# Kernel tuning notes

Hardware: AMD Instinct MI355X
Metric: run time of the kernel (lower is better)

Reference implementation:

```python
import jax, jax.numpy as jnp
import numpy as np

D_MODEL = 1024
N_HEADS = 16
D_K = D_MODEL // N_HEADS
D_FF = 4096
B = 2
T = 2048


def _layernorm(x, gamma, beta, eps=1e-5):
    mu = jnp.mean(x, axis=-1, keepdims=True)
    var = jnp.var(x, axis=-1, keepdims=True)
    return (x - mu) * jax.lax.rsqrt(var + eps) * gamma + beta


def _attention(q_in, kv_in, Wq, bq, Wk, bk, Wv, bv, mask):
    # q_in: [B,Tq,D], kv_in: [B,Tk,D]; Wq/Wk/Wv: [H,D,d_k]; b*: [H,d_k]
    Q = jnp.einsum('btd,hdk->bhtk', q_in, Wq) + bq[None, :, None, :]
    K = jnp.einsum('bsd,hdk->bhsk', kv_in, Wk) + bk[None, :, None, :]
    V = jnp.einsum('bsd,hdk->bhsk', kv_in, Wv) + bv[None, :, None, :]
    scores = jnp.einsum('bhtk,bhsk->bhts', Q, K) / jnp.sqrt(jnp.asarray(D_K, Q.dtype))
    if mask is not None:
        scores = jnp.where(mask, scores, jnp.finfo(scores.dtype).min)
    attn = jax.nn.softmax(scores, axis=-1)
    out = jnp.einsum('bhts,bhsk->bhtk', attn, V)  # [B,H,Tq,d_k]
    # concat heads: [B,Tq,H*d_k] == [B,Tq,D]
    return out.transpose(0, 2, 1, 3).reshape(q_in.shape[0], q_in.shape[1], -1)


def setup_inputs() -> dict:
    key = jax.random.key(0)
    ks = jax.random.split(key, 24)
    s = 0.02
    inp = {
        'dec_input': jax.random.normal(ks[0], (B, T, D_MODEL), jnp.float32),
        'enc_output': jax.random.normal(ks[1], (B, T, D_MODEL), jnp.float32),
        # self-attention per-head weights stacked over heads
        'Wq_s': jax.random.normal(ks[2], (N_HEADS, D_MODEL, D_K), jnp.float32) * s,
        'bq_s': jnp.zeros((N_HEADS, D_K), jnp.float32),
        'Wk_s': jax.random.normal(ks[3], (N_HEADS, D_MODEL, D_K), jnp.float32) * s,
        'bk_s': jnp.zeros((N_HEADS, D_K), jnp.float32),
        'Wv_s': jax.random.normal(ks[4], (N_HEADS, D_MODEL, D_K), jnp.float32) * s,
        'bv_s': jnp.zeros((N_HEADS, D_K), jnp.float32),
        'Wo_s': jax.random.normal(ks[5], (D_MODEL, D_MODEL), jnp.float32) * s,
        'bo_s': jnp.zeros((D_MODEL,), jnp.float32),
        # cross-attention per-head weights
        'Wq_c': jax.random.normal(ks[6], (N_HEADS, D_MODEL, D_K), jnp.float32) * s,
        'bq_c': jnp.zeros((N_HEADS, D_K), jnp.float32),
        'Wk_c': jax.random.normal(ks[7], (N_HEADS, D_MODEL, D_K), jnp.float32) * s,
        'bk_c': jnp.zeros((N_HEADS, D_K), jnp.float32),
        'Wv_c': jax.random.normal(ks[8], (N_HEADS, D_MODEL, D_K), jnp.float32) * s,
        'bv_c': jnp.zeros((N_HEADS, D_K), jnp.float32),
        'Wo_c': jax.random.normal(ks[9], (D_MODEL, D_MODEL), jnp.float32) * s,
        'bo_c': jnp.zeros((D_MODEL,), jnp.float32),
        # FFN
        'W1': jax.random.normal(ks[10], (D_MODEL, D_FF), jnp.float32) * s,
        'b1': jnp.zeros((D_FF,), jnp.float32),
        'W2': jax.random.normal(ks[11], (D_FF, D_MODEL), jnp.float32) * s,
        'b2': jnp.zeros((D_MODEL,), jnp.float32),
        # layernorms
        'g1': jnp.ones((D_MODEL,), jnp.float32), 'be1': jnp.zeros((D_MODEL,), jnp.float32),
        'g2': jnp.ones((D_MODEL,), jnp.float32), 'be2': jnp.zeros((D_MODEL,), jnp.float32),
        'g3': jnp.ones((D_MODEL,), jnp.float32), 'be3': jnp.zeros((D_MODEL,), jnp.float32),
    }
    return inp


def reference(dec_input, enc_output,
              Wq_s, bq_s, Wk_s, bk_s, Wv_s, bv_s, Wo_s, bo_s,
              Wq_c, bq_c, Wk_c, bk_c, Wv_c, bv_c, Wo_c, bo_c,
              W1, b1, W2, b2, g1, be1, g2, be2, g3, be3):
    Tq = dec_input.shape[1]
    causal = jnp.tril(jnp.ones((Tq, Tq), bool))[None, None, :, :]  # [1,1,T,T]
    # masked multi-head self-attention (dropout is identity in eval)
    sa = _attention(dec_input, dec_input, Wq_s, bq_s, Wk_s, bk_s, Wv_s, bv_s, causal)
    sa = sa @ Wo_s.T if False else jnp.einsum('btd,ed->bte', sa, Wo_s.T) if False else sa @ Wo_s + bo_s
    x1 = _layernorm(dec_input + sa, g1, be1)
    # cross-attention (no mask)
    ca = _attention(x1, enc_output, Wq_c, bq_c, Wk_c, bk_c, Wv_c, bv_c, None)
    ca = ca @ Wo_c + bo_c
    x2 = _layernorm(x1 + ca, g2, be2)
    # FFN
    ffn = jax.nn.relu(x2 @ W1 + b1) @ W2 + b2
    x3 = _layernorm(x2 + ffn, g3, be3)
    return x3
```

## Files before the change

kernel.cpp:

```cpp
#include <hip/hip_runtime.h>
#include <hip/hip_bf16.h>

typedef __attribute__((ext_vector_type(8))) short short8;
typedef __attribute__((ext_vector_type(4))) short short4v;
typedef __attribute__((ext_vector_type(4))) float floatx4;

#define TDIM 2048
#define BDIM 2
#define MROWS (BDIM * TDIM)

#define ASM_VMCNT0() __asm__ volatile("s_waitcnt vmcnt(0)" ::: "memory")
#define ASM_LGKM0()  __asm__ volatile("s_waitcnt lgkmcnt(0)" ::: "memory")
#define ASM_BARRIER() __asm__ volatile("s_barrier" ::: "memory")

__device__ __forceinline__ floatx4 mfma16(short4v a, short4v b, floatx4 c) {
#if defined(__HIP_DEVICE_COMPILE__)
#if __has_builtin(__builtin_amdgcn_mfma_f32_16x16x16bf16_1k)
    return __builtin_amdgcn_mfma_f32_16x16x16bf16_1k(a, b, c, 0, 0, 0);
#else
    short8 az = {a[0], a[1], a[2], a[3], 0, 0, 0, 0};
    short8 bz = {b[0], b[1], b[2], b[3], 0, 0, 0, 0};
    return __builtin_amdgcn_mfma_f32_16x16x32_bf16(az, bz, c, 0, 0, 0);
#endif
#else
    (void)a; (void)b;
    return c;
#endif
}

__device__ __forceinline__ void gload_lds16(const void* g, void* l) {
    __builtin_amdgcn_global_load_lds((const __attribute__((address_space(1))) void*)g,
                                     (__attribute__((address_space(3))) void*)l, 16, 0, 0);
}

__device__ __forceinline__ short bf16s(float x) {
    __hip_bfloat16 h = __float2bfloat16(x);
    return *(short*)&h;
}

__global__ __launch_bounds__(256) void cast2_k(const float* __restrict__ a,
                                               const float* __restrict__ b,
                                               __hip_bfloat16* __restrict__ oa,
                                               __hip_bfloat16* __restrict__ ob) {
    const int blk = blockIdx.x;
    const float* in = (blk < 4096) ? a : b;
    __hip_bfloat16* out = (blk < 4096) ? oa : ob;
    const size_t base = (size_t)(blk & 4095) * 1024 + threadIdx.x * 4;
    float4 v = *(const float4*)&in[base];
    out[base + 0] = __float2bfloat16(v.x);
    out[base + 1] = __float2bfloat16(v.y);
    out[base + 2] = __float2bfloat16(v.z);
    out[base + 3] = __float2bfloat16(v.w);
}

__device__ __forceinline__ void t32(float (*tile)[33], const float* __restrict__ in,
                                    __hip_bfloat16* __restrict__ out, int R, int C,
                                    int c0, int r0) {
    const int tx = threadIdx.x & 31, ty = threadIdx.x >> 5;
#pragma unroll
    for (int i = 0; i < 4; ++i)
        tile[ty + 8 * i][tx] = in[(size_t)(r0 + ty + 8 * i) * C + c0 + tx];
    __syncthreads();
#pragma unroll
    for (int i = 0; i < 4; ++i)
        out[(size_t)(c0 + ty + 8 * i) * R + r0 + tx] = __float2bfloat16(tile[tx][ty + 8 * i]);
}

__global__ __launch_bounds__(256) void prep_w_k(
    const float* __restrict__ Wq_s, const float* __restrict__ Wk_s, const float* __restrict__ Wv_s,
    const float* __restrict__ Wq_c, const float* __restrict__ Wk_c, const float* __restrict__ Wv_c,
    const float* __restrict__ Wo_s, const float* __restrict__ Wo_c,
    const float* __restrict__ W1, const float* __restrict__ W2,
    const float* __restrict__ bq_s, const float* __restrict__ bk_s, const float* __restrict__ bv_s,
    const float* __restrict__ bk_c, const float* __restrict__ bv_c,
    __hip_bfloat16* __restrict__ WtQKVs, __hip_bfloat16* __restrict__ WtQc,
    __hip_bfloat16* __restrict__ WtKVc, __hip_bfloat16* __restrict__ WtOs,
    __hip_bfloat16* __restrict__ WtOc, __hip_bfloat16* __restrict__ Wt1,
    __hip_bfloat16* __restrict__ Wt2,
    float* __restrict__ BiasQKVs, float* __restrict__ BiasKVc) {
    __shared__ float tile[32][33];
    const int t = blockIdx.x;
    if (t < 6144) {
        const int seg = t >> 10, tl = t & 1023;
        const float* s;
        __hip_bfloat16* d;
        if (seg == 0) { s = Wq_s; d = WtQKVs; }
        else if (seg == 1) { s = Wk_s; d = WtQKVs + 1048576; }
        else if (seg == 2) { s = Wv_s; d = WtQKVs + 2097152; }
        else if (seg == 3) { s = Wq_c; d = WtQc; }
        else if (seg == 4) { s = Wk_c; d = WtKVc; }
        else { s = Wv_c; d = WtKVc + 1048576; }
        const int slab = tl >> 6, rem = tl & 63;
        t32(tile, s + (size_t)slab * 65536, d + (size_t)slab * 65536, 1024, 64,
            (rem & 1) * 32, (rem >> 1) * 32);
    } else if (t < 8192) {
        const int rem = (t - 6144) & 1023;
        const float* s = (t < 7168) ? Wo_s : Wo_c;
        __hip_bfloat16* d = (t < 7168) ? WtOs : WtOc;
        t32(tile, s, d, 1024, 1024, (rem & 31) * 32, (rem >> 5) * 32);
    } else if (t < 12288) {
        const int rem = t - 8192;
        t32(tile, W1, Wt1, 1024, 4096, (rem & 127) * 32, (rem >> 7) * 32);
    } else if (t < 16384) {
        const int rem = t - 12288;
        t32(tile, W2, Wt2, 4096, 1024, (rem & 31) * 32, (rem >> 5) * 32);
    } else if (t < 16396) {
        const int i = (t - 16384) * 256 + threadIdx.x;
        BiasQKVs[i] = (i < 1024) ? bq_s[i] : (i < 2048 ? bk_s[i - 1024] : bv_s[i - 2048]);
    } else {
        const int i = (t - 16396) * 256 + threadIdx.x;
        BiasKVc[i] = (i < 1024) ? bk_c[i] : bv_c[i - 1024];
    }
}

__device__ __forceinline__ void gemm_core(
    const __hip_bfloat16* __restrict__ A, const __hip_bfloat16* __restrict__ Bt,
    int K, int kBeg, int kLen,
    const float* __restrict__ bias, __hip_bfloat16* __restrict__ C, int ldc,
    float* __restrict__ Pf,
    __hip_bfloat16* __restrict__ Vt, int vt_col0, int relu,
    int m0, int n0, __hip_bfloat16* sm) {
    const int tid = threadIdx.x;
    const int lane = tid & 63, wave = tid >> 6;
    const int quad = lane >> 4, l16 = lane & 15;
    const int wm = (wave >> 1) * 64, wn = (wave & 1) * 64;
    const int lrow = lane >> 3;
    const int gsw = (((lane & 7) ^ lrow)) * 8;
    const int sw7 = l16 & 7;
    const __hip_bfloat16* gA = A + (size_t)(m0 + wave * 32 + lrow) * K + kBeg + gsw;
    const __hip_bfloat16* gB = Bt + (size_t)(n0 + wave * 32 + lrow) * K + kBeg + gsw;
    __hip_bfloat16* lA = sm + wave * 2048;
    __hip_bfloat16* lB = sm + 16384 + wave * 2048;
    floatx4 acc[4][4] = {};
    const int T = kLen >> 6;
#pragma unroll
    for (int i = 0; i < 4; ++i) {
        gload_lds16(gA + (size_t)i * 8 * K, lA + i * 512);
        gload_lds16(gB + (size_t)i * 8 * K, lB + i * 512);
    }
    for (int t = 0; t < T; ++t) {
        ASM_VMCNT0();
        ASM_BARRIER();
        if (t + 1 < T) {
            const int koff = (t + 1) << 6;
            const int b = ((t + 1) & 1) * 8192;
#pragma unroll
            for (int i = 0; i < 4; ++i) {
                gload_lds16(gA + (size_t)i * 8 * K + koff, lA + b + i * 512);
                gload_lds16(gB + (size_t)i * 8 * K + koff, lB + b + i * 512);
            }
        }
        const __hip_bfloat16* cA = sm + (t & 1) * 8192;
        const __hip_bfloat16* cB = sm + 16384 + (t & 1) * 8192;
#pragma unroll
        for (int kc = 0; kc < 2; ++kc) {
            short8 af[4], bfr[4];
#pragma unroll
            for (int i = 0; i < 4; ++i) {
                af[i] = *(const short8*)&cA[(wm + i * 16 + l16) * 64 +
                                            (((kc * 4 + quad) ^ sw7) * 8)];
                bfr[i] = *(const short8*)&cB[(wn + i * 16 + l16) * 64 +
                                             (((kc * 4 + quad) ^ sw7) * 8)];
            }
#pragma unroll
            for (int mi = 0; mi < 4; ++mi)
#pragma unroll
                for (int ni = 0; ni < 4; ++ni)
                    acc[mi][ni] =
                        __builtin_amdgcn_mfma_f32_16x16x32_bf16(af[mi], bfr[ni], acc[mi][ni], 0, 0, 0);
        }
    }
    if (Pf) {
#pragma unroll
        for (int ni = 0; ni < 4; ++ni) {
            const int col = n0 + wn + ni * 16 + l16;
#pragma unroll
            for (int mi = 0; mi < 4; ++mi)
#pragma unroll
                for (int r = 0; r < 4; ++r) {
                    const int row = m0 + wm + mi * 16 + quad * 4 + r;
                    Pf[(size_t)row * ldc + col] = acc[mi][ni][r];
                }
        }
    } else {
        const bool toVt = (n0 >= vt_col0);
#pragma unroll
        for (int ni = 0; ni < 4; ++ni) {
            const int col = n0 + wn + ni * 16 + l16;
            const float bv = bias[col];
#pragma unroll
            for (int mi = 0; mi < 4; ++mi) {
                const int row0 = m0 + wm + mi * 16 + quad * 4;
                if (toVt) {
                    const int b = row0 >> 11, t0 = row0 & (TDIM - 1);
                    short4v pk;
#pragma unroll
                    for (int r = 0; r < 4; ++r) pk[r] = bf16s(acc[mi][ni][r] + bv);
                    *(short4v*)&Vt[((size_t)(b * 1024 + (col - vt_col0)) << 11) + t0] = pk;
                } else {
#pragma unroll
                    for (int r = 0; r < 4; ++r) {
                        float v = acc[mi][ni][r] + bv;
                        if (relu) v = fmaxf(v, 0.f);
                        C[(size_t)(row0 + r) * ldc + col] = __float2bfloat16(v);
                    }
                }
            }
        }
    }
}

__global__ __launch_bounds__(256) void gemm_bf16_k(const __hip_bfloat16* __restrict__ A,
                                                   const __hip_bfloat16* __restrict__ Bt,
                                                   const float* __restrict__ bias,
                                                   __hip_bfloat16* __restrict__ C,
                                                   int N, int K, int relu,
                                                   __hip_bfloat16* __restrict__ Vt, int vt_col0) {
    __shared__ __hip_bfloat16 sm[2 * 128 * 64 * 2];
    gemm_core(A, Bt, K, 0, K, bias, C, N, nullptr, Vt, vt_col0, relu,
              blockIdx.y * 128, blockIdx.x * 128, sm);
}

__global__ __launch_bounds__(256) void gemm_sk2_k(const __hip_bfloat16* __restrict__ A,
                                                  const __hip_bfloat16* __restrict__ Bt,
                                                  float* __restrict__ Pf, int N, int K) {
    __shared__ __hip_bfloat16 sm[2 * 128 * 64 * 2];
    const int z = blockIdx.z;
    gemm_core(A, Bt, K, z * (K >> 1), K >> 1, nullptr, nullptr, N,
              Pf + (size_t)z * MROWS * N, nullptr, 1 << 30, 0,
              blockIdx.y * 128, blockIdx.x * 128, sm);
}

__global__ __launch_bounds__(256) void gemm_pair_k(
    const __hip_bfloat16* __restrict__ A1, const __hip_bfloat16* __restrict__ Bt1,
    const float* __restrict__ bias1, __hip_bfloat16* __restrict__ C1, int N1, int K1,
    const __hip_bfloat16* __restrict__ A2, const __hip_bfloat16* __restrict__ Bt2,
    const float* __restrict__ bias2, __hip_bfloat16* __restrict__ C2, int N2, int K2,
    __hip_bfloat16* __restrict__ Vt2, int vtc2, int nx1) {
    __shared__ __hip_bfloat16 sm[2 * 128 * 64 * 2];
    if ((int)blockIdx.x < nx1)
        gemm_core(A1, Bt1, K1, 0, K1, bias1, C1, N1, nullptr, nullptr, 1 << 30, 0,
                  blockIdx.y * 128, blockIdx.x * 128, sm);
    else
        gemm_core(A2, Bt2, K2, 0, K2, bias2, C2, N2, nullptr, Vt2, vtc2, 0,
                  blockIdx.y * 128, (blockIdx.x - nx1) * 128, sm);
}

__device__ __forceinline__ void flash_one(
    const __hip_bfloat16* __restrict__ Q, int ldq, int qc0,
    const __hip_bfloat16* __restrict__ Kp, int ldk,
    const __hip_bfloat16* __restrict__ Vp,
    __hip_bfloat16* __restrict__ O, int causal, int q0, size_t rowb, int h,
    __hip_bfloat16* sK, __hip_bfloat16* sV) {
    const int tid = threadIdx.x, lane = tid & 63, wave = tid >> 6;
    const int quad = lane >> 4, l16 = lane & 15;
    const int lrow = lane >> 3;
    const int gsw = ((lane & 7) ^ lrow) * 8;
    const int sw7 = l16 & 7;
    short8 qf[2];
    {
        const __hip_bfloat16* qp = Q + (rowb + q0 + wave * 16 + l16) * (size_t)ldq + qc0 + h * 64;
        const float qs = 0.18033688f;
        short8 r0 = *(const short8*)(qp + quad * 8);
        short8 r1 = *(const short8*)(qp + 32 + quad * 8);
#pragma unroll
        for (int j = 0; j < 8; ++j) {
            qf[0][j] = bf16s(__uint_as_float(((unsigned)(unsigned short)r0[j]) << 16) * qs);
            qf[1][j] = bf16s(__uint_as_float(((unsigned)(unsigned short)r1[j]) << 16) * qs);
        }
    }
    short4v ones4;
#pragma unroll
    for (int j = 0; j < 4; ++j) ones4[j] = (short)0x3F80;
    floatx4 Ot[4] = {};
    floatx4 accl = {};
    const int nDiag = q0 >> 6;
    const int lastT = causal ? nDiag : (TDIM >> 6) - 1;
    ASM_LGKM0();
    ASM_BARRIER();
#pragma unroll
    for (int i = 0; i < 2; ++i) {
        const int rb = wave * 16 + i * 8;
        gload_lds16(&Kp[(rowb + rb + lrow) * (size_t)ldk + gsw], &sK[rb * 64]);
        gload_lds16(&Vp[(size_t)(rb + lrow) * TDIM + gsw], &sV[rb * 64]);
    }
    for (int t = 0; t <= lastT; ++t) {
        ASM_VMCNT0();
        ASM_BARRIER();
        if (t < lastT) {
            const int s1 = (t + 1) << 6, nb = ((t + 1) & 1) * 4096;
#pragma unroll
            for (int i = 0; i < 2; ++i) {
                const int rb = wave * 16 + i * 8;
                gload_lds16(&Kp[(rowb + s1 + rb + lrow) * (size_t)ldk + gsw], &sK[nb + rb * 64]);
                gload_lds16(&Vp[(size_t)(rb + lrow) * TDIM + s1 + gsw], &sV[nb + rb * 64]);
            }
        }
        const int cb = (t & 1) * 4096;
        floatx4 Sf[4] = {};
#pragma unroll
        for (int st = 0; st < 4; ++st) {
            short8 b0 = *(const short8*)&sK[cb + (st * 16 + l16) * 64 + ((quad ^ sw7) * 8)];
            short8 b1 = *(const short8*)&sK[cb + (st * 16 + l16) * 64 + (((4 + quad) ^ sw7) * 8)];
            Sf[st] = __builtin_amdgcn_mfma_f32_16x16x32_bf16(b0, qf[0], Sf[st], 0, 0, 0);
            Sf[st] = __builtin_amdgcn_mfma_f32_16x16x32_bf16(b1, qf[1], Sf[st], 0, 0, 0);
        }
#pragma unroll
        for (int st = 0; st < 4; ++st)
#pragma unroll
            for (int r = 0; r < 4; ++r) Sf[st][r] = exp2f(Sf[st][r]);
        if (causal && t == nDiag) {
            const int qr = wave * 16 + l16;
#pragma unroll
            for (int st = 0; st < 4; ++st)
#pragma unroll
                for (int r = 0; r < 4; ++r)
                    if (st * 16 + quad * 4 + r > qr) Sf[st][r] = 0.f;
        }
        short4v pf[4];
#pragma unroll
        for (int st = 0; st < 4; ++st)
#pragma unroll
            for (int r = 0; r < 4; ++r) pf[st][r] = bf16s(Sf[st][r]);
#pragma unroll
        for (int st = 0; st < 4; ++st) accl = mfma16(ones4, pf[st], accl);
#pragma unroll
        for (int dt = 0; dt < 4; ++dt)
#pragma unroll
            for (int st = 0; st < 4; ++st) {
                short4v av = *(const short4v*)&sV[cb + (dt * 16 + l16) * 64 +
                                                 (((st * 2 + (quad >> 1)) ^ sw7) * 8) +
                                                 (quad & 1) * 4];
                Ot[dt] = mfma16(av, pf[st], Ot[dt]);
            }
    }
    const float inv = 1.0f / accl[0];
    __hip_bfloat16* op = O + (rowb + q0 + wave * 16 + l16) * (size_t)1024 + h * 64 + quad * 4;
#pragma unroll
    for (int dt = 0; dt < 4; ++dt) {
        short4v pk;
#pragma unroll
        for (int r = 0; r < 4; ++r) pk[r] = bf16s(Ot[dt][r] * inv);
        *(short4v*)(op + dt * 16) = pk;
    }
}

__global__ __launch_bounds__(256) void flash_attn(const __hip_bfloat16* __restrict__ Q, int ldq, int qc0,
                                                  const __hip_bfloat16* __restrict__ K, int ldk, int kc0,
                                                  const __hip_bfloat16* __restrict__ Vt,
                                                  __hip_bfloat16* __restrict__ O, int causal) {
    __shared__ __hip_bfloat16 sK[2 * 64 * 64];
    __shared__ __hip_bfloat16 sV[2 * 64 * 64];
    const int bh = blockIdx.y, b = bh >> 4, h = bh & 15;
    const size_t rowb = (size_t)b * TDIM;
    const __hip_bfloat16* Kp = K + kc0 + h * 64;
    const __hip_bfloat16* Vp = Vt + ((size_t)(b * 1024 + h * 64) << 11);
    if (causal) {
        flash_one(Q, ldq, qc0, Kp, ldk, Vp, O, 1, (31 - (int)blockIdx.x) * 64, rowb, h, sK, sV);
    } else {
        flash_one(Q, ldq, qc0, Kp, ldk, Vp, O, 0, (int)blockIdx.x * 64, rowb, h, sK, sV);
    }
}

__global__ __launch_bounds__(256) void ln2_k(const float* __restrict__ resid,
                                             const float* __restrict__ d0,
                                             const float* __restrict__ d1,
                                             const float* __restrict__ biasN,
                                             const float* __restrict__ gamma,
                                             const float* __restrict__ beta,
                                             float* __restrict__ outf,
                                             __hip_bfloat16* __restrict__ outb) {
    const int row = blockIdx.x, tid = threadIdx.x;
    const size_t base = (size_t)row * 1024;
    float x[4], s = 0.f, sq = 0.f;
#pragma unroll
    for (int i = 0; i < 4; ++i) {
        const int c = tid + 256 * i;
        x[i] = resid[base + c] + d0[base + c] + d1[base + c] + biasN[c];
        s += x[i];
        sq += x[i] * x[i];
    }
#pragma unroll
    for (int off = 32; off > 0; off >>= 1) {
        s += __shfl_down(s, off);
        sq += __shfl_down(sq, off);
    }
    __shared__ float red[8];
    if ((tid & 63) == 0) {
        red[tid >> 6] = s;
        red[4 + (tid >> 6)] = sq;
    }
    __syncthreads();
    const float S = red[0] + red[1] + red[2] + red[3];
    const float Q2 = red[4] + red[5] + red[6] + red[7];
    const float mean = S * (1.f / 1024.f);
    const float var = Q2 * (1.f / 1024.f) - mean * mean;
    const float rstd = rsqrtf(var + 1e-5f);
#pragma unroll
    for (int i = 0; i < 4; ++i) {
        const int c = tid + 256 * i;
        const float y = (x[i] - mean) * rstd * gamma[c] + beta[c];
        outf[base + c] = y;
        if (outb) outb[base + c] = __float2bfloat16(y);
    }
}

extern "C" void kernel_launch(void* const* d_in, const int* in_sizes, int n_in,
                              void* d_out, int out_size, void* d_ws, size_t ws_size,
                              hipStream_t stream) {
    (void)in_sizes; (void)n_in; (void)out_size; (void)ws_size;
    const float* dec  = (const float*)d_in[0];
    const float* enc  = (const float*)d_in[1];
    const float* Wq_s = (const float*)d_in[2];
    const float* bq_s = (const float*)d_in[3];
    const float* Wk_s = (const float*)d_in[4];
    const float* bk_s = (const float*)d_in[5];
    const float* Wv_s = (const float*)d_in[6];
    const float* bv_s = (const float*)d_in[7];
    const float* Wo_s = (const float*)d_in[8];
    const float* bo_s = (const float*)d_in[9];
    const float* Wq_c = (const float*)d_in[10];
    const float* bq_c = (const float*)d_in[11];
    const float* Wk_c = (const float*)d_in[12];
    const float* bk_c = (const float*)d_in[13];
    const float* Wv_c = (const float*)d_in[14];
    const float* bv_c = (const float*)d_in[15];
    const float* Wo_c = (const float*)d_in[16];
    const float* bo_c = (const float*)d_in[17];
    const float* W1   = (const float*)d_in[18];
    const float* b1   = (const float*)d_in[19];
    const float* W2   = (const float*)d_in[20];
    const float* b2   = (const float*)d_in[21];
    const float* g1   = (const float*)d_in[22];
    const float* be1  = (const float*)d_in[23];
    const float* g2   = (const float*)d_in[24];
    const float* be2  = (const float*)d_in[25];
    const float* g3   = (const float*)d_in[26];
    const float* be3  = (const float*)d_in[27];

    char* w = (char*)d_ws;
    const size_t MB = 1ull << 20;
    __hip_bfloat16* Xdec   = (__hip_bfloat16*)(w + 0 * MB);
    __hip_bfloat16* Xenc   = (__hip_bfloat16*)(w + 8 * MB);
    __hip_bfloat16* WtQKVs = (__hip_bfloat16*)(w + 16 * MB);
    __hip_bfloat16* WtOs   = (__hip_bfloat16*)(w + 22 * MB);
    __hip_bfloat16* WtQc   = (__hip_bfloat16*)(w + 24 * MB);
    __hip_bfloat16* WtKVc  = (__hip_bfloat16*)(w + 26 * MB);
    __hip_bfloat16* WtOc   = (__hip_bfloat16*)(w + 30 * MB);
    __hip_bfloat16* Wt1    = (__hip_bfloat16*)(w + 32 * MB);
    __hip_bfloat16* Wt2    = (__hip_bfloat16*)(w + 40 * MB);
    float*          BiasQKVs = (float*)(w + 48 * MB);
    float*          BiasKVc  = (float*)(w + 48 * MB + 65536);
    __hip_bfloat16* QKV    = (__hip_bfloat16*)(w + 49 * MB);
    __hip_bfloat16* Qc     = QKV;
    __hip_bfloat16* KVc    = (__hip_bfloat16*)(w + 57 * MB);
    float*          Psplit = (float*)(w + 49 * MB);
    __hip_bfloat16* VtBuf  = (__hip_bfloat16*)(w + 73 * MB);
    __hip_bfloat16* Attn   = (__hip_bfloat16*)(w + 81 * MB);
    float*          X1f    = (float*)(w + 97 * MB);
    __hip_bfloat16* X1b    = (__hip_bfloat16*)(w + 113 * MB);
    float*          X2f    = (float*)(w + 121 * MB);
    __hip_bfloat16* X2b    = (__hip_bfloat16*)(w + 137 * MB);
    __hip_bfloat16* H1     = (__hip_bfloat16*)(w + 145 * MB);
    float*          P0     = Psplit;
    float*          P1     = Psplit + (size_t)MROWS * 1024;
    const int NOVT = 1 << 30;

    cast2_k<<<8192, 256, 0, stream>>>(dec, enc, Xdec, Xenc);
    prep_w_k<<<16404, 256, 0, stream>>>(Wq_s, Wk_s, Wv_s, Wq_c, Wk_c, Wv_c, Wo_s, Wo_c,
                                        W1, W2, bq_s, bk_s, bv_s, bk_c, bv_c,
                                        WtQKVs, WtQc, WtKVc, WtOs, WtOc, Wt1, Wt2,
                                        BiasQKVs, BiasKVc);

    gemm_bf16_k<<<dim3(24, 32), 256, 0, stream>>>(Xdec, WtQKVs, BiasQKVs, QKV, 3072, 1024, 0,
                                                  VtBuf, 2048);
    flash_attn<<<dim3(32, 32), 256, 0, stream>>>(QKV, 3072, 0, QKV, 3072, 1024, VtBuf, Attn, 1);
    gemm_sk2_k<<<dim3(8, 32, 2), 256, 0, stream>>>(Attn, WtOs, Psplit, 1024, 1024);
    ln2_k<<<MROWS, 256, 0, stream>>>(dec, P0, P1, bo_s, g1, be1, X1f, X1b);

    gemm_pair_k<<<dim3(24, 32), 256, 0, stream>>>(X1b, WtQc, bq_c, Qc, 1024, 1024,
                                                  Xenc, WtKVc, BiasKVc, KVc, 2048, 1024,
                                                  VtBuf, 1024, 8);
    flash_attn<<<dim3(32, 32), 256, 0, stream>>>(Qc, 1024, 0, KVc, 2048, 0, VtBuf, Attn, 0);
    gemm_sk2_k<<<dim3(8, 32, 2), 256, 0, stream>>>(Attn, WtOc, Psplit, 1024, 1024);
    ln2_k<<<MROWS, 256, 0, stream>>>(X1f, P0, P1, bo_c, g2, be2, X2f, X2b);

    gemm_bf16_k<<<dim3(32, 32), 256, 0, stream>>>(X2b, Wt1, b1, H1, 4096, 1024, 1,
                                                  (__hip_bfloat16*)nullptr, NOVT);
    gemm_sk2_k<<<dim3(8, 32, 2), 256, 0, stream>>>(H1, Wt2, Psplit, 1024, 4096);
    ln2_k<<<MROWS, 256, 0, stream>>>(X2f, P0, P1, b2, g3, be3, (float*)d_out, (__hip_bfloat16*)nullptr);
}
```

Measured before the change: 553.5 us.

## Split long causal attention query tiles across two blocks with combine kernel

For causal self-attention, query tiles 16..31 (the longest KV ranges) are each split into two halves of the KV loop, run as separate blocks writing fp32 partial outputs and row sums, then merged by a new combine kernel. This balances per-block work across the grid (48 blocks per head instead of 32) to cut the tail of the causal triangle. It also swaps exp2f for the hardware exp2 builtin. The cost is extra partial-buffer traffic and an additional kernel launch. The split needs no max rescaling because the softmax here is unnormalised and uses no running max.

```diff
diff --git a/kernel.cpp b/kernel.cpp
--- a/kernel.cpp
+++ b/kernel.cpp
@@ -36,6 +36,18 @@
 __device__ __forceinline__ short bf16s(float x) {
     __hip_bfloat16 h = __float2bfloat16(x);
     return *(short*)&h;
+}
+
+__device__ __forceinline__ float fexp2(float x) {
+#if defined(__HIP_DEVICE_COMPILE__)
+#if __has_builtin(__builtin_amdgcn_exp2f)
+    return __builtin_amdgcn_exp2f(x);
+#else
+    return exp2f(x);
+#endif
+#else
+    return x;
+#endif
 }
 
 __global__ __launch_bounds__(256) void cast2_k(const float* __restrict__ a,
@@ -251,6 +263,7 @@
     const __hip_bfloat16* __restrict__ Kp, int ldk,
     const __hip_bfloat16* __restrict__ Vp,
     __hip_bfloat16* __restrict__ O, int causal, int q0, size_t rowb, int h,
+    int tBeg, int tEnd, float* __restrict__ Opart, float* __restrict__ lpart,
     __hip_bfloat16* sK, __hip_bfloat16* sV) {
     const int tid = threadIdx.x, lane = tid & 63, wave = tid >> 6;
     const int quad = lane >> 4, l16 = lane & 15;
@@ -275,19 +288,21 @@
     floatx4 Ot[4] = {};
     floatx4 accl = {};
     const int nDiag = q0 >> 6;
-    const int lastT = causal ? nDiag : (TDIM >> 6) - 1;
     ASM_LGKM0();
     ASM_BARRIER();
-#pragma unroll
-    for (int i = 0; i < 2; ++i) {
-        const int rb = wave * 16 + i * 8;
-        gload_lds16(&Kp[(rowb + rb + lrow) * (size_t)ldk + gsw], &sK[rb * 64]);
-        gload_lds16(&Vp[(size_t)(rb + lrow) * TDIM + gsw], &sV[rb * 64]);
-    }
-    for (int t = 0; t <= lastT; ++t) {
+    {
+        const int s0 = tBeg << 6, pb = (tBeg & 1) * 4096;
+#pragma unroll
+        for (int i = 0; i < 2; ++i) {
+            const int rb = wave * 16 + i * 8;
+            gload_lds16(&Kp[(rowb + s0 + rb + lrow) * (size_t)ldk + gsw], &sK[pb + rb * 64]);
+            gload_lds16(&Vp[(size_t)(rb + lrow) * TDIM + s0 + gsw], &sV[pb + rb * 64]);
+        }
+    }
+    for (int t = tBeg; t < tEnd; ++t) {
         ASM_VMCNT0();
         ASM_BARRIER();
-        if (t < lastT) {
+        if (t + 1 < tEnd) {
             const int s1 = (t + 1) << 6, nb = ((t + 1) & 1) * 4096;
 #pragma unroll
             for (int i = 0; i < 2; ++i) {
@@ -308,7 +323,7 @@
 #pragma unroll
         for (int st = 0; st < 4; ++st)
 #pragma unroll
-            for (int r = 0; r < 4; ++r) Sf[st][r] = exp2f(Sf[st][r]);
+            for (int r = 0; r < 4; ++r) Sf[st][r] = fexp2(Sf[st][r]);
         if (causal && t == nDiag) {
             const int qr = wave * 16 + l16;
 #pragma unroll
@@ -334,21 +349,31 @@
                 Ot[dt] = mfma16(av, pf[st], Ot[dt]);
             }
     }
-    const float inv = 1.0f / accl[0];
-    __hip_bfloat16* op = O + (rowb + q0 + wave * 16 + l16) * (size_t)1024 + h * 64 + quad * 4;
-#pragma unroll
-    for (int dt = 0; dt < 4; ++dt) {
-        short4v pk;
-#pragma unroll
-        for (int r = 0; r < 4; ++r) pk[r] = bf16s(Ot[dt][r] * inv);
-        *(short4v*)(op + dt * 16) = pk;
+    if (Opart) {
+        const int qrow = wave * 16 + l16;
+#pragma unroll
+        for (int dt = 0; dt < 4; ++dt)
+            *(floatx4*)&Opart[qrow * 64 + dt * 16 + quad * 4] = Ot[dt];
+        if (quad == 0) lpart[qrow] = accl[0];
+    } else {
+        const float inv = 1.0f / accl[0];
+        __hip_bfloat16* op = O + (rowb + q0 + wave * 16 + l16) * (size_t)1024 + h * 64 + quad * 4;
+#pragma unroll
+        for (int dt = 0; dt < 4; ++dt) {
+            short4v pk;
+#pragma unroll
+            for (int r = 0; r < 4; ++r) pk[r] = bf16s(Ot[dt][r] * inv);
+            *(short4v*)(op + dt * 16) = pk;
+        }
     }
 }
 
 __global__ __launch_bounds__(256) void flash_attn(const __hip_bfloat16* __restrict__ Q, int ldq, int qc0,
                                                   const __hip_bfloat16* __restrict__ K, int ldk, int kc0,
                                                   const __hip_bfloat16* __restrict__ Vt,
-                                                  __hip_bfloat16* __restrict__ O, int causal) {
+                                                  __hip_bfloat16* __restrict__ O, int causal,
+                                                  float* __restrict__ Opart,
+                                                  float* __restrict__ lpart) {
     __shared__ __hip_bfloat16 sK[2 * 64 * 64];
     __shared__ __hip_bfloat16 sV[2 * 64 * 64];
     const int bh = blockIdx.y, b = bh >> 4, h = bh & 15;
@@ -356,9 +381,46 @@
     const __hip_bfloat16* Kp = K + kc0 + h * 64;
     const __hip_bfloat16* Vp = Vt + ((size_t)(b * 1024 + h * 64) << 11);
     if (causal) {
-        flash_one(Q, ldq, qc0, Kp, ldk, Vp, O, 1, (31 - (int)blockIdx.x) * 64, rowb, h, sK, sV);
+        const int bx = blockIdx.x;
+        if (bx < 32) {
+            const int i = 16 + (bx >> 1), hh = bx & 1;
+            const int n = i + 1, n2 = n >> 1;
+            const int p = bh * 16 + (i - 16);
+            float* Op = Opart + (size_t)p * 8192 + hh * 4096;
+            float* lp = lpart + p * 128 + hh * 64;
+            flash_one(Q, ldq, qc0, Kp, ldk, Vp, O, 1, i * 64, rowb, h,
+                      hh ? n2 : 0, hh ? n : n2, Op, lp, sK, sV);
+        } else {
+            const int i = 47 - bx;
+            flash_one(Q, ldq, qc0, Kp, ldk, Vp, O, 1, i * 64, rowb, h,
+                      0, i + 1, nullptr, nullptr, sK, sV);
+        }
     } else {
-        flash_one(Q, ldq, qc0, Kp, ldk, Vp, O, 0, (int)blockIdx.x * 64, rowb, h, sK, sV);
+        flash_one(Q, ldq, qc0, Kp, ldk, Vp, O, 0, (int)blockIdx.x * 64, rowb, h,
+                  0, TDIM >> 6, nullptr, nullptr, sK, sV);
+    }
+}
+
+__global__ __launch_bounds__(256) void fa_combine_k(const float* __restrict__ Opart,
+                                                    const float* __restrict__ lpart,
+                                                    __hip_bfloat16* __restrict__ O) {
+    const int p = blockIdx.x;
+    const int bh = p >> 4, i = (p & 15) + 16;
+    const int b = bh >> 4, h = bh & 15;
+    const int tid = threadIdx.x;
+    const int q = tid >> 2, dseg = (tid & 3) * 16;
+    const float* O0 = Opart + (size_t)p * 8192;
+    const float* O1 = O0 + 4096;
+    const float inv = 1.f / (lpart[p * 128 + q] + lpart[p * 128 + 64 + q]);
+    __hip_bfloat16* op = O + ((size_t)(b * TDIM) + i * 64 + q) * 1024 + h * 64 + dseg;
+#pragma unroll
+    for (int j = 0; j < 4; ++j) {
+        floatx4 a = *(const floatx4*)&O0[q * 64 + dseg + j * 4];
+        floatx4 c = *(const floatx4*)&O1[q * 64 + dseg + j * 4];
+        short4v pk;
+#pragma unroll
+        for (int r = 0; r < 4; ++r) pk[r] = bf16s((a[r] + c[r]) * inv);
+        *(short4v*)(op + j * 4) = pk;
     }
 }
 
@@ -462,6 +524,8 @@
     float*          X2f    = (float*)(w + 121 * MB);
     __hip_bfloat16* X2b    = (__hip_bfloat16*)(w + 137 * MB);
     __hip_bfloat16* H1     = (__hip_bfloat16*)(w + 145 * MB);
+    float*          FaO    = (float*)(w + 145 * MB);
+    float*          FaL    = (float*)(w + 161 * MB);
     float*          P0     = Psplit;
     float*          P1     = Psplit + (size_t)MROWS * 1024;
     const int NOVT = 1 << 30;
@@ -474,14 +538,17 @@
 
     gemm_bf16_k<<<dim3(24, 32), 256, 0, stream>>>(Xdec, WtQKVs, BiasQKVs, QKV, 3072, 1024, 0,
                                                   VtBuf, 2048);
-    flash_attn<<<dim3(32, 32), 256, 0, stream>>>(QKV, 3072, 0, QKV, 3072, 1024, VtBuf, Attn, 1);
+    flash_attn<<<dim3(48, 32), 256, 0, stream>>>(QKV, 3072, 0, QKV, 3072, 1024, VtBuf, Attn, 1,
+                                                 FaO, FaL);
+    fa_combine_k<<<512, 256, 0, stream>>>(FaO, FaL, Attn);
     gemm_sk2_k<<<dim3(8, 32, 2), 256, 0, stream>>>(Attn, WtOs, Psplit, 1024, 1024);
     ln2_k<<<MROWS, 256, 0, stream>>>(dec, P0, P1, bo_s, g1, be1, X1f, X1b);
 
     gemm_pair_k<<<dim3(24, 32), 256, 0, stream>>>(X1b, WtQc, bq_c, Qc, 1024, 1024,
                                                   Xenc, WtKVc, BiasKVc, KVc, 2048, 1024,
                                                   VtBuf, 1024, 8);
-    flash_attn<<<dim3(32, 32), 256, 0, stream>>>(Qc, 1024, 0, KVc, 2048, 0, VtBuf, Attn, 0);
+    flash_attn<<<dim3(32, 32), 256, 0, stream>>>(Qc, 1024, 0, KVc, 2048, 0, VtBuf, Attn, 0,
+                                                 nullptr, nullptr);
     gemm_sk2_k<<<dim3(8, 32, 2), 256, 0, stream>>>(Attn, WtOc, Psplit, 1024, 1024);
     ln2_k<<<MROWS, 256, 0, stream>>>(X1f, P0, P1, bo_c, g2, be2, X2f, X2b);
 
```

New measurement: 527.1 us. 1.05x faster.
